# Kernel tuning notes

Hardware: AMD Instinct MI355X
Metric: run time of the kernel (lower is better)

## Reference

```python
import jax, jax.numpy as jnp
import numpy as np

N = 8192      # number of graph nodes (superpixels)
C = 128       # input_dim
OUT = 128     # output_dim
T = 256       # theta_1 projection dim
EPS = 1e-5    # BatchNorm1d eps (default)
NEG = -9e15   # zero_vec fill value from the torch code
SLOPE = 0.01  # LeakyReLU default negative slope


def setup_inputs() -> dict:
    key = jax.random.key(0)
    k = jax.random.split(key, 6)
    H = jax.random.normal(k[0], (N, C), dtype=jnp.float32)
    A = (jax.random.uniform(k[1], (N, N)) < 0.01).astype(jnp.float32)
    gamma = jnp.ones((C,), jnp.float32)
    beta = jnp.zeros((C,), jnp.float32)
    W1 = jax.random.normal(k[2], (C, T), dtype=jnp.float32) * 0.05
    b1 = jnp.zeros((T,), jnp.float32)
    Wo = jax.random.normal(k[3], (C, OUT), dtype=jnp.float32) * 0.05
    bo = jnp.zeros((OUT,), jnp.float32)
    return {"H": H, "A": A, "gamma": gamma, "beta": beta,
            "W1": W1, "b1": b1, "Wo": Wo, "bo": bo}


def _leaky(x):
    return jnp.where(x >= 0, x, SLOPE * x)


def reference(H, A, gamma, beta, W1, b1, Wo, bo):
    # BatchNorm1d (training-mode batch statistics, biased variance)
    mu = H.mean(axis=0)
    var = H.var(axis=0)
    Hn = (H - mu) * jax.lax.rsqrt(var + EPS) * gamma + beta   # [N, C]

    # theta_1 projection and dense pairwise similarity
    Hx = Hn @ W1 + b1                                          # [N, T]
    e = jax.nn.sigmoid(Hx @ Hx.T)                              # [N, N]

    mask = jnp.ceil(A * 1e-5)                                  # 1 where A>0
    A1 = jnp.where(mask > 0, e, jnp.float32(NEG))              # [N, N]

    # model == 'normal' -> no clamp branch
    A_soft = jax.nn.softmax(A1 + jnp.eye(N, dtype=A1.dtype), axis=1)

    HW = Hn @ Wo + bo                                          # [N, OUT]
    out1 = _leaky(A_soft @ HW)
    A1_soft = jax.nn.softmax(A1, axis=1)
    out2 = _leaky(A1_soft @ HW)
    return (out1 + out2, A_soft)
```

## Files before the change

### kernel.cpp

```cpp
#include <hip/hip_runtime.h>


#define NN    8192
#define CC    128
#define TT    256
#define OUTD  128
#define FD    384
#define CAP   256

#define WS_STATS  8
#define WS_PARAMS 264
#define WS_BCAT   520
#define WS_WCAT   904
#define WS_F      50176

typedef unsigned int v4u __attribute__((ext_vector_type(4)));

__device__ __forceinline__ float b2f(unsigned short u) {
    return __uint_as_float(((unsigned int)u) << 16);
}
__device__ __forceinline__ unsigned short f2b(float f) {
    unsigned int x = __float_as_uint(f);
    return (unsigned short)((x + 0x7fffu + ((x >> 16) & 1u)) >> 16);
}
__device__ __forceinline__ int pick_gamma(const void* g0, const void* g1, const void* g2) {
    if (*(const unsigned int*)g0 == 0x3F800000u) return 0;
    if (*(const unsigned int*)g1 == 0x3F800000u) return 1;
    if (*(const unsigned int*)g2 == 0x3F800000u) return 2;
    return 0;
}

__global__ __launch_bounds__(384) void k_init(const float* __restrict__ W1,
                                              const float* __restrict__ b1,
                                              const float* __restrict__ Wo,
                                              const void* g0, const void* g1, const void* g2,
                                              float* __restrict__ ws) {
    int t = threadIdx.x, b = blockIdx.x;
    if (b < 128) {
        ws[WS_WCAT + b * FD + t] = (t < TT) ? W1[(size_t)b * TT + t]
                                            : Wo[(size_t)b * OUTD + (t - TT)];
    } else {
        if (t < 256) ws[WS_STATS + t] = 0.0f;
        int gs = pick_gamma(g0, g1, g2);
        const float* cand[3] = {(const float*)g0, (const float*)g1, (const float*)g2};
        const float* bo = cand[gs == 2 ? 1 : 2];
        ws[WS_BCAT + t] = (t < TT) ? b1[t] : bo[t - TT];
    }
}

__global__ __launch_bounds__(256) void k_stats(const float* __restrict__ H,
                                               float* __restrict__ ws) {
    __shared__ float ssum[256], ssq[256];
    int tid = threadIdx.x;
    int c = tid & 127, rh = tid >> 7;
    int r0 = blockIdx.x * 64;
    float s = 0.0f, q = 0.0f;
#pragma unroll 8
    for (int k = 0; k < 32; ++k) {
        float v = H[(size_t)(r0 + rh + 2 * k) * CC + c];
        s += v; q += v * v;
    }
    ssum[tid] = s; ssq[tid] = q;
    __syncthreads();
    if (tid < 128) {
        atomicAdd(&ws[WS_STATS + c],       ssum[tid] + ssum[tid + 128]);
        atomicAdd(&ws[WS_STATS + 128 + c], ssq[tid]  + ssq[tid + 128]);
    }
}

__global__ __launch_bounds__(128) void k_final(const void* g0, const void* g1, const void* g2,
                                               float* __restrict__ ws) {
    int gs = pick_gamma(g0, g1, g2);
    const float* cand[3] = {(const float*)g0, (const float*)g1, (const float*)g2};
    const float* gamma = cand[gs];
    const float* beta  = cand[gs == 0 ? 1 : 0];
    int c = threadIdx.x;
    float mu  = ws[WS_STATS + c] * (1.0f / NN);
    float var = ws[WS_STATS + 128 + c] * (1.0f / NN) - mu * mu;
    float rs  = rsqrtf(var + 1e-5f);
    float sc  = gamma[c] * rs;
    ws[WS_PARAMS + c]       = sc;
    ws[WS_PARAMS + 128 + c] = beta[c] - mu * sc;
}

__global__ __launch_bounds__(256) void k_gemm(const float* __restrict__ H,
                                              float* __restrict__ ws) {
    __shared__ float As[64][65];
    __shared__ float Bs[64][64];
    const float* params = ws + WS_PARAMS;
    const float* Wcat   = ws + WS_WCAT;
    const float* bcat   = ws + WS_BCAT;
    unsigned short* F   = (unsigned short*)(ws + WS_F);
    int tid = threadIdx.x;
    int m0 = blockIdx.x * 64, n0 = blockIdx.y * 64;
    int ty = tid >> 4, tx = tid & 15;
    float acc[4][4];
#pragma unroll
    for (int m = 0; m < 4; ++m)
#pragma unroll
        for (int n = 0; n < 4; ++n) acc[m][n] = 0.0f;

    for (int ks = 0; ks < CC; ks += 64) {
#pragma unroll
        for (int it = 0; it < 16; ++it) {
            int idx = tid + it * 256;
            int r = idx >> 6, k = idx & 63;
            As[r][k] = H[(size_t)(m0 + r) * CC + ks + k] * params[ks + k]
                     + params[128 + ks + k];
        }
#pragma unroll
        for (int it = 0; it < 16; ++it) {
            int idx = tid + it * 256;
            int k = idx >> 6, n = idx & 63;
            Bs[k][n] = Wcat[(ks + k) * FD + n0 + n];
        }
        __syncthreads();
#pragma unroll
        for (int k = 0; k < 64; ++k) {
            float4 b4 = *(const float4*)&Bs[k][tx * 4];
            float a0 = As[ty * 4 + 0][k];
            float a1 = As[ty * 4 + 1][k];
            float a2 = As[ty * 4 + 2][k];
            float a3 = As[ty * 4 + 3][k];
            acc[0][0] += a0 * b4.x; acc[0][1] += a0 * b4.y; acc[0][2] += a0 * b4.z; acc[0][3] += a0 * b4.w;
            acc[1][0] += a1 * b4.x; acc[1][1] += a1 * b4.y; acc[1][2] += a1 * b4.z; acc[1][3] += a1 * b4.w;
            acc[2][0] += a2 * b4.x; acc[2][1] += a2 * b4.y; acc[2][2] += a2 * b4.z; acc[2][3] += a2 * b4.w;
            acc[3][0] += a3 * b4.x; acc[3][1] += a3 * b4.y; acc[3][2] += a3 * b4.z; acc[3][3] += a3 * b4.w;
        }
        __syncthreads();
    }
#pragma unroll
    for (int n = 0; n < 4; ++n) {
        int gn = n0 + tx * 4 + n;
        float bias = bcat[gn];
#pragma unroll
        for (int m = 0; m < 4; ++m) {
            int gm = m0 + ty * 4 + m;
            F[(size_t)gm * FD + gn] = f2b(acc[m][n] + bias);
        }
    }
}

__global__ __launch_bounds__(256, 8) void k_sattn(const float* __restrict__ A,
                                                  float* __restrict__ ws,
                                                  float* __restrict__ outO,
                                                  float* __restrict__ outAs) {
    __shared__ __align__(16) float hxi[TT];
    __shared__ unsigned short nbr[CAP];
    __shared__ float ev1[CAP];
    __shared__ float ev2[CAP];
    __shared__ float po1[256], po2[256];
    __shared__ int   cnt;
    __shared__ float s1, s2;

    const unsigned short* F = (const unsigned short*)(ws + WS_F);
    int tid = threadIdx.x;
    int i = blockIdx.x;

    const v4u* arow = (const v4u*)(A + (size_t)i * NN);
    v4u r[8];
#pragma unroll
    for (int q = 0; q < 8; ++q) r[q] = arow[tid + 256 * q];

    hxi[tid] = b2f(F[(size_t)i * FD + tid]);
    if (tid == 0) { cnt = 0; s1 = 0.0f; s2 = 0.0f; }
    __syncthreads();

#pragma unroll
    for (int q = 0; q < 8; ++q) {
        if (r[q].x | r[q].y | r[q].z | r[q].w) {
            int base = (tid + 256 * q) * 4;
            if (r[q].x) { int p = atomicAdd(&cnt, 1); if (p < CAP) nbr[p] = (unsigned short)(base + 0); }
            if (r[q].y) { int p = atomicAdd(&cnt, 1); if (p < CAP) nbr[p] = (unsigned short)(base + 1); }
            if (r[q].z) { int p = atomicAdd(&cnt, 1); if (p < CAP) nbr[p] = (unsigned short)(base + 2); }
            if (r[q].w) { int p = atomicAdd(&cnt, 1); if (p < CAP) nbr[p] = (unsigned short)(base + 3); }
        }
    }
    __syncthreads();
    int cn = cnt < CAP ? cnt : CAP;

    int wave = tid >> 6, lane = tid & 63;
    float4 x4 = ((const float4*)hxi)[lane];
    for (int p0 = wave; p0 < cn; p0 += 16) {
        int pp0 = p0, pp1 = p0 + 4, pp2 = p0 + 8, pp3 = p0 + 12;
        ushort4 h0, h1, h2, h3;
        h0 = ((const ushort4*)(F + (size_t)nbr[pp0] * FD))[lane];
        if (pp1 < cn) h1 = ((const ushort4*)(F + (size_t)nbr[pp1] * FD))[lane];
        if (pp2 < cn) h2 = ((const ushort4*)(F + (size_t)nbr[pp2] * FD))[lane];
        if (pp3 < cn) h3 = ((const ushort4*)(F + (size_t)nbr[pp3] * FD))[lane];
        float d0 = b2f(h0.x) * x4.x + b2f(h0.y) * x4.y + b2f(h0.z) * x4.z + b2f(h0.w) * x4.w;
        float d1 = (pp1 < cn) ? b2f(h1.x) * x4.x + b2f(h1.y) * x4.y + b2f(h1.z) * x4.z + b2f(h1.w) * x4.w : 0.0f;
        float d2 = (pp2 < cn) ? b2f(h2.x) * x4.x + b2f(h2.y) * x4.y + b2f(h2.z) * x4.z + b2f(h2.w) * x4.w : 0.0f;
        float d3 = (pp3 < cn) ? b2f(h3.x) * x4.x + b2f(h3.y) * x4.y + b2f(h3.z) * x4.z + b2f(h3.w) * x4.w : 0.0f;
#pragma unroll
        for (int off = 32; off >= 1; off >>= 1) {
            d0 += __shfl_xor(d0, off, 64);
            d1 += __shfl_xor(d1, off, 64);
            d2 += __shfl_xor(d2, off, 64);
            d3 += __shfl_xor(d3, off, 64);
        }
        if (lane == 0) {
            ev1[pp0] = 1.0f / (1.0f + __expf(-d0));
            if (pp1 < cn) ev1[pp1] = 1.0f / (1.0f + __expf(-d1));
            if (pp2 < cn) ev1[pp2] = 1.0f / (1.0f + __expf(-d2));
            if (pp3 < cn) ev1[pp3] = 1.0f / (1.0f + __expf(-d3));
        }
    }
    __syncthreads();

    float l1 = 0.0f, l2 = 0.0f;
    if (tid < cn) {
        float e  = ev1[tid];
        float eb = __expf(e);
        float a1 = ((int)nbr[tid] == i) ? eb * 2.7182818284590452f : eb;
        ev1[tid] = a1; ev2[tid] = eb;
        l1 = a1; l2 = eb;
    }
#pragma unroll
    for (int off = 32; off >= 1; off >>= 1) {
        l1 += __shfl_xor(l1, off, 64);
        l2 += __shfl_xor(l2, off, 64);
    }
    if (lane == 0) { atomicAdd(&s1, l1); atomicAdd(&s2, l2); }
    __syncthreads();

    float inv1 = (s1 > 0.0f) ? 1.0f / s1 : 0.0f;
    float inv2 = (s2 > 0.0f) ? 1.0f / s2 : 0.0f;

    if (tid < cn) outAs[(size_t)i * NN + nbr[tid]] = ev1[tid] * inv1;

    {
        int half = tid >> 7;
        int c = tid & 127;
        const unsigned short* Fhw = F + TT + c;
        float a1 = 0.0f, a2 = 0.0f;
#pragma unroll 8
        for (int p = half; p < cn; p += 2) {
            float h = b2f(Fhw[(size_t)nbr[p] * FD]);
            a1 += ev1[p] * h;
            a2 += ev2[p] * h;
        }
        po1[tid] = a1; po2[tid] = a2;
    }
    __syncthreads();
    if (tid < OUTD) {
        float o1 = (po1[tid] + po1[tid + 128]) * inv1;
        float o2 = (po2[tid] + po2[tid + 128]) * inv2;
        o1 = (o1 >= 0.0f) ? o1 : 0.01f * o1;
        o2 = (o2 >= 0.0f) ? o2 : 0.01f * o2;
        outO[(size_t)i * OUTD + tid] = o1 + o2;
    }
}

extern "C" void kernel_launch(void* const* d_in, const int* in_sizes, int n_in,
                              void* d_out, int out_size, void* d_ws, size_t ws_size,
                              hipStream_t stream) {
    int iH = -1, iA = -1, iW1 = -1, iWo = -1, ib1 = -1, i128[3] = {-1, -1, -1};
    int n128 = 0;
    bool ok = (n_in == 8);
    if (ok) {
        for (int i = 0; i < 8; ++i) {
            int s = in_sizes[i];
            if      (s == 67108864 && iA  < 0) iA  = i;
            else if (s == 1048576  && iH  < 0) iH  = i;
            else if (s == 32768    && iW1 < 0) iW1 = i;
            else if (s == 16384    && iWo < 0) iWo = i;
            else if (s == 256      && ib1 < 0) ib1 = i;
            else if (s == 128      && n128 < 3) i128[n128++] = i;
            else { ok = false; break; }
        }
        if (iA < 0 || iH < 0 || iW1 < 0 || iWo < 0 || ib1 < 0 || n128 != 3) ok = false;
    }
    if (!ok) { iH = 0; iA = 1; i128[0] = 2; i128[1] = 3; iW1 = 4; ib1 = 5; iWo = 6; i128[2] = 7; }

    const float* H  = (const float*)d_in[iH];
    const float* A  = (const float*)d_in[iA];
    const float* W1 = (const float*)d_in[iW1];
    const float* b1 = (const float*)d_in[ib1];
    const float* Wo = (const float*)d_in[iWo];
    const void*  g0 = d_in[i128[0]];
    const void*  g1 = d_in[i128[1]];
    const void*  g2 = d_in[i128[2]];

    float* outO  = (float*)d_out;
    float* outAs = outO + (size_t)NN * OUTD;
    float* ws    = (float*)d_ws;

    k_init <<<129, 384, 0, stream>>>(W1, b1, Wo, g0, g1, g2, ws);
    k_stats<<<128, 256, 0, stream>>>(H, ws);
    k_final<<<1, 128, 0, stream>>>(g0, g1, g2, ws);
    k_gemm <<<dim3(128, 6), 256, 0, stream>>>(H, ws);
    hipMemsetAsync(outAs, 0, (size_t)NN * NN * sizeof(float), stream);
    k_sattn<<<NN, 256, 0, stream>>>(A, ws, outO, outAs);
}
```

Baseline: 528.9 us.

## Process four rows per block and prefetch next adjacency row during compute

The attention kernel now handles four consecutive rows per block instead of one, with a grid of N/4 blocks. Right after building the neighbour list for the current row, it issues the loads of the next row of A, so that 32KB read overlaps the gather and dot-product phase. The cost is fewer blocks (2048), an extra barrier per row, and registers held live across the loop, which can reduce overlap from occupancy. The kernel is likely dominated by streaming the 256MB A matrix and memsetting outAs, so the gain depends on whether per-block latency was the limit.

```diff
diff --git a/kernel.cpp b/kernel.cpp
--- a/kernel.cpp
+++ b/kernel.cpp
@@ -7,6 +7,8 @@
 #define OUTD  128
 #define FD    384
 #define CAP   256
+#define RPB   4
+#define GRID  (NN / RPB)
 
 #define WS_STATS  8
 #define WS_PARAMS 264
@@ -155,100 +157,112 @@
 
     const unsigned short* F = (const unsigned short*)(ws + WS_F);
     int tid = threadIdx.x;
-    int i = blockIdx.x;
-
-    const v4u* arow = (const v4u*)(A + (size_t)i * NN);
+    int base = blockIdx.x * RPB;
+
     v4u r[8];
-#pragma unroll
-    for (int q = 0; q < 8; ++q) r[q] = arow[tid + 256 * q];
-
-    hxi[tid] = b2f(F[(size_t)i * FD + tid]);
-    if (tid == 0) { cnt = 0; s1 = 0.0f; s2 = 0.0f; }
-    __syncthreads();
-
-#pragma unroll
-    for (int q = 0; q < 8; ++q) {
-        if (r[q].x | r[q].y | r[q].z | r[q].w) {
-            int base = (tid + 256 * q) * 4;
-            if (r[q].x) { int p = atomicAdd(&cnt, 1); if (p < CAP) nbr[p] = (unsigned short)(base + 0); }
-            if (r[q].y) { int p = atomicAdd(&cnt, 1); if (p < CAP) nbr[p] = (unsigned short)(base + 1); }
-            if (r[q].z) { int p = atomicAdd(&cnt, 1); if (p < CAP) nbr[p] = (unsigned short)(base + 2); }
-            if (r[q].w) { int p = atomicAdd(&cnt, 1); if (p < CAP) nbr[p] = (unsigned short)(base + 3); }
-        }
-    }
-    __syncthreads();
-    int cn = cnt < CAP ? cnt : CAP;
-
-    int wave = tid >> 6, lane = tid & 63;
-    float4 x4 = ((const float4*)hxi)[lane];
-    for (int p0 = wave; p0 < cn; p0 += 16) {
-        int pp0 = p0, pp1 = p0 + 4, pp2 = p0 + 8, pp3 = p0 + 12;
-        ushort4 h0, h1, h2, h3;
-        h0 = ((const ushort4*)(F + (size_t)nbr[pp0] * FD))[lane];
-        if (pp1 < cn) h1 = ((const ushort4*)(F + (size_t)nbr[pp1] * FD))[lane];
-        if (pp2 < cn) h2 = ((const ushort4*)(F + (size_t)nbr[pp2] * FD))[lane];
-        if (pp3 < cn) h3 = ((const ushort4*)(F + (size_t)nbr[pp3] * FD))[lane];
-        float d0 = b2f(h0.x) * x4.x + b2f(h0.y) * x4.y + b2f(h0.z) * x4.z + b2f(h0.w) * x4.w;
-        float d1 = (pp1 < cn) ? b2f(h1.x) * x4.x + b2f(h1.y) * x4.y + b2f(h1.z) * x4.z + b2f(h1.w) * x4.w : 0.0f;
-        float d2 = (pp2 < cn) ? b2f(h2.x) * x4.x + b2f(h2.y) * x4.y + b2f(h2.z) * x4.z + b2f(h2.w) * x4.w : 0.0f;
-        float d3 = (pp3 < cn) ? b2f(h3.x) * x4.x + b2f(h3.y) * x4.y + b2f(h3.z) * x4.z + b2f(h3.w) * x4.w : 0.0f;
+    {
+        const v4u* a0 = (const v4u*)(A + (size_t)base * NN);
+#pragma unroll
+        for (int q = 0; q < 8; ++q) r[q] = a0[tid + 256 * q];
+    }
+
+    for (int rr = 0; rr < RPB; ++rr) {
+        int i = base + rr;
+        if (tid == 0) { cnt = 0; s1 = 0.0f; s2 = 0.0f; }
+        hxi[tid] = b2f(F[(size_t)i * FD + tid]);
+        __syncthreads();
+
+#pragma unroll
+        for (int q = 0; q < 8; ++q) {
+            if (r[q].x | r[q].y | r[q].z | r[q].w) {
+                int bpos = (tid + 256 * q) * 4;
+                if (r[q].x) { int p = atomicAdd(&cnt, 1); if (p < CAP) nbr[p] = (unsigned short)(bpos + 0); }
+                if (r[q].y) { int p = atomicAdd(&cnt, 1); if (p < CAP) nbr[p] = (unsigned short)(bpos + 1); }
+                if (r[q].z) { int p = atomicAdd(&cnt, 1); if (p < CAP) nbr[p] = (unsigned short)(bpos + 2); }
+                if (r[q].w) { int p = atomicAdd(&cnt, 1); if (p < CAP) nbr[p] = (unsigned short)(bpos + 3); }
+            }
+        }
+        __syncthreads();
+        int cn = cnt < CAP ? cnt : CAP;
+
+        if (rr + 1 < RPB) {
+            const v4u* an = (const v4u*)(A + (size_t)(i + 1) * NN);
+#pragma unroll
+            for (int q = 0; q < 8; ++q) r[q] = an[tid + 256 * q];
+        }
+
+        int wave = tid >> 6, lane = tid & 63;
+        float4 x4 = ((const float4*)hxi)[lane];
+        for (int p0 = wave; p0 < cn; p0 += 16) {
+            int pp1 = p0 + 4, pp2 = p0 + 8, pp3 = p0 + 12;
+            ushort4 h0, h1, h2, h3;
+            h0 = ((const ushort4*)(F + (size_t)nbr[p0] * FD))[lane];
+            if (pp1 < cn) h1 = ((const ushort4*)(F + (size_t)nbr[pp1] * FD))[lane];
+            if (pp2 < cn) h2 = ((const ushort4*)(F + (size_t)nbr[pp2] * FD))[lane];
+            if (pp3 < cn) h3 = ((const ushort4*)(F + (size_t)nbr[pp3] * FD))[lane];
+            float d0 = b2f(h0.x) * x4.x + b2f(h0.y) * x4.y + b2f(h0.z) * x4.z + b2f(h0.w) * x4.w;
+            float d1 = (pp1 < cn) ? b2f(h1.x) * x4.x + b2f(h1.y) * x4.y + b2f(h1.z) * x4.z + b2f(h1.w) * x4.w : 0.0f;
+            float d2 = (pp2 < cn) ? b2f(h2.x) * x4.x + b2f(h2.y) * x4.y + b2f(h2.z) * x4.z + b2f(h2.w) * x4.w : 0.0f;
+            float d3 = (pp3 < cn) ? b2f(h3.x) * x4.x + b2f(h3.y) * x4.y + b2f(h3.z) * x4.z + b2f(h3.w) * x4.w : 0.0f;
+#pragma unroll
+            for (int off = 32; off >= 1; off >>= 1) {
+                d0 += __shfl_xor(d0, off, 64);
+                d1 += __shfl_xor(d1, off, 64);
+                d2 += __shfl_xor(d2, off, 64);
+                d3 += __shfl_xor(d3, off, 64);
+            }
+            if (lane == 0) {
+                ev1[p0] = 1.0f / (1.0f + __expf(-d0));
+                if (pp1 < cn) ev1[pp1] = 1.0f / (1.0f + __expf(-d1));
+                if (pp2 < cn) ev1[pp2] = 1.0f / (1.0f + __expf(-d2));
+                if (pp3 < cn) ev1[pp3] = 1.0f / (1.0f + __expf(-d3));
+            }
+        }
+        __syncthreads();
+
+        float l1 = 0.0f, l2 = 0.0f;
+        if (tid < cn) {
+            float e  = ev1[tid];
+            float eb = __expf(e);
+            float a1 = ((int)nbr[tid] == i) ? eb * 2.7182818284590452f : eb;
+            ev1[tid] = a1; ev2[tid] = eb;
+            l1 = a1; l2 = eb;
+        }
 #pragma unroll
         for (int off = 32; off >= 1; off >>= 1) {
-            d0 += __shfl_xor(d0, off, 64);
-            d1 += __shfl_xor(d1, off, 64);
-            d2 += __shfl_xor(d2, off, 64);
-            d3 += __shfl_xor(d3, off, 64);
-        }
-        if (lane == 0) {
-            ev1[pp0] = 1.0f / (1.0f + __expf(-d0));
-            if (pp1 < cn) ev1[pp1] = 1.0f / (1.0f + __expf(-d1));
-            if (pp2 < cn) ev1[pp2] = 1.0f / (1.0f + __expf(-d2));
-            if (pp3 < cn) ev1[pp3] = 1.0f / (1.0f + __expf(-d3));
-        }
-    }
-    __syncthreads();
-
-    float l1 = 0.0f, l2 = 0.0f;
-    if (tid < cn) {
-        float e  = ev1[tid];
-        float eb = __expf(e);
-        float a1 = ((int)nbr[tid] == i) ? eb * 2.7182818284590452f : eb;
-        ev1[tid] = a1; ev2[tid] = eb;
-        l1 = a1; l2 = eb;
-    }
-#pragma unroll
-    for (int off = 32; off >= 1; off >>= 1) {
-        l1 += __shfl_xor(l1, off, 64);
-        l2 += __shfl_xor(l2, off, 64);
-    }
-    if (lane == 0) { atomicAdd(&s1, l1); atomicAdd(&s2, l2); }
-    __syncthreads();
-
-    float inv1 = (s1 > 0.0f) ? 1.0f / s1 : 0.0f;
-    float inv2 = (s2 > 0.0f) ? 1.0f / s2 : 0.0f;
-
-    if (tid < cn) outAs[(size_t)i * NN + nbr[tid]] = ev1[tid] * inv1;
-
-    {
-        int half = tid >> 7;
-        int c = tid & 127;
-        const unsigned short* Fhw = F + TT + c;
-        float a1 = 0.0f, a2 = 0.0f;
+            l1 += __shfl_xor(l1, off, 64);
+            l2 += __shfl_xor(l2, off, 64);
+        }
+        if (lane == 0) { atomicAdd(&s1, l1); atomicAdd(&s2, l2); }
+        __syncthreads();
+
+        float inv1 = (s1 > 0.0f) ? 1.0f / s1 : 0.0f;
+        float inv2 = (s2 > 0.0f) ? 1.0f / s2 : 0.0f;
+
+        if (tid < cn) outAs[(size_t)i * NN + nbr[tid]] = ev1[tid] * inv1;
+
+        {
+            int half = tid >> 7;
+            int c = tid & 127;
+            const unsigned short* Fhw = F + TT + c;
+            float a1 = 0.0f, a2 = 0.0f;
 #pragma unroll 8
-        for (int p = half; p < cn; p += 2) {
-            float h = b2f(Fhw[(size_t)nbr[p] * FD]);
-            a1 += ev1[p] * h;
-            a2 += ev2[p] * h;
-        }
-        po1[tid] = a1; po2[tid] = a2;
-    }
-    __syncthreads();
-    if (tid < OUTD) {
-        float o1 = (po1[tid] + po1[tid + 128]) * inv1;
-        float o2 = (po2[tid] + po2[tid + 128]) * inv2;
-        o1 = (o1 >= 0.0f) ? o1 : 0.01f * o1;
-        o2 = (o2 >= 0.0f) ? o2 : 0.01f * o2;
-        outO[(size_t)i * OUTD + tid] = o1 + o2;
+            for (int p = half; p < cn; p += 2) {
+                float h = b2f(Fhw[(size_t)nbr[p] * FD]);
+                a1 += ev1[p] * h;
+                a2 += ev2[p] * h;
+            }
+            po1[tid] = a1; po2[tid] = a2;
+        }
+        __syncthreads();
+        if (tid < OUTD) {
+            float o1 = (po1[tid] + po1[tid + 128]) * inv1;
+            float o2 = (po2[tid] + po2[tid + 128]) * inv2;
+            o1 = (o1 >= 0.0f) ? o1 : 0.01f * o1;
+            o2 = (o2 >= 0.0f) ? o2 : 0.01f * o2;
+            outO[(size_t)i * OUTD + tid] = o1 + o2;
+        }
+        __syncthreads();
     }
 }
 
@@ -291,5 +305,5 @@
     k_final<<<1, 128, 0, stream>>>(g0, g1, g2, ws);
     k_gemm <<<dim3(128, 6), 256, 0, stream>>>(H, ws);
     hipMemsetAsync(outAs, 0, (size_t)NN * NN * sizeof(float), stream);
-    k_sattn<<<NN, 256, 0, stream>>>(A, ws, outO, outAs);
-}
+    k_sattn<<<GRID, 256, 0, stream>>>(A, ws, outO, outAs);
+}
```

After: 623.8 us. 17.9% more time.

## Process one graph row per wavefront in sparse attention kernel

Applied to the files above, without the earlier changes.

Restructures the sparse attention kernel so each 64-lane wave handles a whole row independently, with four rows per block. This removes the block-wide __syncthreads barriers and shared-memory atomics on the softmax sums, using wave shuffles instead. The weighted aggregation now has each lane produce two output columns with packed 32-bit loads. The trade-off is less parallelism per row, so each wave scans a full 32 KB row of A and walks every neighbor serially, which may lengthen per-row latency.

```diff
diff --git a/kernel.cpp b/kernel.cpp
--- a/kernel.cpp
+++ b/kernel.cpp
@@ -145,53 +145,53 @@
                                                   float* __restrict__ ws,
                                                   float* __restrict__ outO,
                                                   float* __restrict__ outAs) {
-    __shared__ __align__(16) float hxi[TT];
-    __shared__ unsigned short nbr[CAP];
-    __shared__ float ev1[CAP];
-    __shared__ float ev2[CAP];
-    __shared__ float po1[256], po2[256];
-    __shared__ int   cnt;
-    __shared__ float s1, s2;
+    __shared__ unsigned short nbr[4][CAP];
+    __shared__ float ev1[4][CAP];
+    __shared__ float ev2[4][CAP];
+    __shared__ int   cnt[4][16];
 
     const unsigned short* F = (const unsigned short*)(ws + WS_F);
-    int tid = threadIdx.x;
-    int i = blockIdx.x;
+    int tid  = threadIdx.x;
+    int wv   = tid >> 6, lane = tid & 63;
+    int i    = blockIdx.x * 4 + wv;
+
+    ushort4 hx = ((const ushort4*)(F + (size_t)i * FD))[lane];
+    float4 x4;
+    x4.x = b2f(hx.x); x4.y = b2f(hx.y); x4.z = b2f(hx.z); x4.w = b2f(hx.w);
+
+    if (lane == 0) cnt[wv][0] = 0;
 
     const v4u* arow = (const v4u*)(A + (size_t)i * NN);
-    v4u r[8];
-#pragma unroll
-    for (int q = 0; q < 8; ++q) r[q] = arow[tid + 256 * q];
-
-    hxi[tid] = b2f(F[(size_t)i * FD + tid]);
-    if (tid == 0) { cnt = 0; s1 = 0.0f; s2 = 0.0f; }
-    __syncthreads();
-
-#pragma unroll
-    for (int q = 0; q < 8; ++q) {
-        if (r[q].x | r[q].y | r[q].z | r[q].w) {
-            int base = (tid + 256 * q) * 4;
-            if (r[q].x) { int p = atomicAdd(&cnt, 1); if (p < CAP) nbr[p] = (unsigned short)(base + 0); }
-            if (r[q].y) { int p = atomicAdd(&cnt, 1); if (p < CAP) nbr[p] = (unsigned short)(base + 1); }
-            if (r[q].z) { int p = atomicAdd(&cnt, 1); if (p < CAP) nbr[p] = (unsigned short)(base + 2); }
-            if (r[q].w) { int p = atomicAdd(&cnt, 1); if (p < CAP) nbr[p] = (unsigned short)(base + 3); }
-        }
-    }
-    __syncthreads();
-    int cn = cnt < CAP ? cnt : CAP;
-
-    int wave = tid >> 6, lane = tid & 63;
-    float4 x4 = ((const float4*)hxi)[lane];
-    for (int p0 = wave; p0 < cn; p0 += 16) {
-        int pp0 = p0, pp1 = p0 + 4, pp2 = p0 + 8, pp3 = p0 + 12;
+#pragma unroll
+    for (int ch = 0; ch < 4; ++ch) {
+        v4u r[8];
+#pragma unroll
+        for (int q = 0; q < 8; ++q) r[q] = arow[lane + 64 * q + 512 * ch];
+#pragma unroll
+        for (int q = 0; q < 8; ++q) {
+            if (r[q].x | r[q].y | r[q].z | r[q].w) {
+                int base = (lane + 64 * q + 512 * ch) * 4;
+                if (r[q].x) { int p = atomicAdd(&cnt[wv][0], 1); if (p < CAP) nbr[wv][p] = (unsigned short)(base + 0); }
+                if (r[q].y) { int p = atomicAdd(&cnt[wv][0], 1); if (p < CAP) nbr[wv][p] = (unsigned short)(base + 1); }
+                if (r[q].z) { int p = atomicAdd(&cnt[wv][0], 1); if (p < CAP) nbr[wv][p] = (unsigned short)(base + 2); }
+                if (r[q].w) { int p = atomicAdd(&cnt[wv][0], 1); if (p < CAP) nbr[wv][p] = (unsigned short)(base + 3); }
+            }
+        }
+    }
+    int cn = cnt[wv][0];
+    if (cn > CAP) cn = CAP;
+
+    for (int p0 = 0; p0 < cn; p0 += 4) {
+        int p1 = p0 + 1, p2 = p0 + 2, p3 = p0 + 3;
         ushort4 h0, h1, h2, h3;
-        h0 = ((const ushort4*)(F + (size_t)nbr[pp0] * FD))[lane];
-        if (pp1 < cn) h1 = ((const ushort4*)(F + (size_t)nbr[pp1] * FD))[lane];
-        if (pp2 < cn) h2 = ((const ushort4*)(F + (size_t)nbr[pp2] * FD))[lane];
-        if (pp3 < cn) h3 = ((const ushort4*)(F + (size_t)nbr[pp3] * FD))[lane];
+        h0 = ((const ushort4*)(F + (size_t)nbr[wv][p0] * FD))[lane];
+        if (p1 < cn) h1 = ((const ushort4*)(F + (size_t)nbr[wv][p1] * FD))[lane];
+        if (p2 < cn) h2 = ((const ushort4*)(F + (size_t)nbr[wv][p2] * FD))[lane];
+        if (p3 < cn) h3 = ((const ushort4*)(F + (size_t)nbr[wv][p3] * FD))[lane];
         float d0 = b2f(h0.x) * x4.x + b2f(h0.y) * x4.y + b2f(h0.z) * x4.z + b2f(h0.w) * x4.w;
-        float d1 = (pp1 < cn) ? b2f(h1.x) * x4.x + b2f(h1.y) * x4.y + b2f(h1.z) * x4.z + b2f(h1.w) * x4.w : 0.0f;
-        float d2 = (pp2 < cn) ? b2f(h2.x) * x4.x + b2f(h2.y) * x4.y + b2f(h2.z) * x4.z + b2f(h2.w) * x4.w : 0.0f;
-        float d3 = (pp3 < cn) ? b2f(h3.x) * x4.x + b2f(h3.y) * x4.y + b2f(h3.z) * x4.z + b2f(h3.w) * x4.w : 0.0f;
+        float d1 = (p1 < cn) ? b2f(h1.x) * x4.x + b2f(h1.y) * x4.y + b2f(h1.z) * x4.z + b2f(h1.w) * x4.w : 0.0f;
+        float d2 = (p2 < cn) ? b2f(h2.x) * x4.x + b2f(h2.y) * x4.y + b2f(h2.z) * x4.z + b2f(h2.w) * x4.w : 0.0f;
+        float d3 = (p3 < cn) ? b2f(h3.x) * x4.x + b2f(h3.y) * x4.y + b2f(h3.z) * x4.z + b2f(h3.w) * x4.w : 0.0f;
 #pragma unroll
         for (int off = 32; off >= 1; off >>= 1) {
             d0 += __shfl_xor(d0, off, 64);
@@ -200,55 +200,53 @@
             d3 += __shfl_xor(d3, off, 64);
         }
         if (lane == 0) {
-            ev1[pp0] = 1.0f / (1.0f + __expf(-d0));
-            if (pp1 < cn) ev1[pp1] = 1.0f / (1.0f + __expf(-d1));
-            if (pp2 < cn) ev1[pp2] = 1.0f / (1.0f + __expf(-d2));
-            if (pp3 < cn) ev1[pp3] = 1.0f / (1.0f + __expf(-d3));
-        }
-    }
-    __syncthreads();
+            ev1[wv][p0] = 1.0f / (1.0f + __expf(-d0));
+            if (p1 < cn) ev1[wv][p1] = 1.0f / (1.0f + __expf(-d1));
+            if (p2 < cn) ev1[wv][p2] = 1.0f / (1.0f + __expf(-d2));
+            if (p3 < cn) ev1[wv][p3] = 1.0f / (1.0f + __expf(-d3));
+        }
+    }
 
     float l1 = 0.0f, l2 = 0.0f;
-    if (tid < cn) {
-        float e  = ev1[tid];
+    for (int p = lane; p < cn; p += 64) {
+        float e  = ev1[wv][p];
         float eb = __expf(e);
-        float a1 = ((int)nbr[tid] == i) ? eb * 2.7182818284590452f : eb;
-        ev1[tid] = a1; ev2[tid] = eb;
-        l1 = a1; l2 = eb;
+        float a1 = ((int)nbr[wv][p] == i) ? eb * 2.7182818284590452f : eb;
+        ev1[wv][p] = a1; ev2[wv][p] = eb;
+        l1 += a1; l2 += eb;
     }
 #pragma unroll
     for (int off = 32; off >= 1; off >>= 1) {
         l1 += __shfl_xor(l1, off, 64);
         l2 += __shfl_xor(l2, off, 64);
     }
-    if (lane == 0) { atomicAdd(&s1, l1); atomicAdd(&s2, l2); }
-    __syncthreads();
-
-    float inv1 = (s1 > 0.0f) ? 1.0f / s1 : 0.0f;
-    float inv2 = (s2 > 0.0f) ? 1.0f / s2 : 0.0f;
-
-    if (tid < cn) outAs[(size_t)i * NN + nbr[tid]] = ev1[tid] * inv1;
+    float inv1 = (l1 > 0.0f) ? 1.0f / l1 : 0.0f;
+    float inv2 = (l2 > 0.0f) ? 1.0f / l2 : 0.0f;
+
+    for (int p = lane; p < cn; p += 64) {
+        outAs[(size_t)i * NN + nbr[wv][p]] = ev1[wv][p] * inv1;
+    }
 
     {
-        int half = tid >> 7;
-        int c = tid & 127;
-        const unsigned short* Fhw = F + TT + c;
-        float a1 = 0.0f, a2 = 0.0f;
-#pragma unroll 8
-        for (int p = half; p < cn; p += 2) {
-            float h = b2f(Fhw[(size_t)nbr[p] * FD]);
-            a1 += ev1[p] * h;
-            a2 += ev2[p] * h;
-        }
-        po1[tid] = a1; po2[tid] = a2;
-    }
-    __syncthreads();
-    if (tid < OUTD) {
-        float o1 = (po1[tid] + po1[tid + 128]) * inv1;
-        float o2 = (po2[tid] + po2[tid + 128]) * inv2;
-        o1 = (o1 >= 0.0f) ? o1 : 0.01f * o1;
-        o2 = (o2 >= 0.0f) ? o2 : 0.01f * o2;
-        outO[(size_t)i * OUTD + tid] = o1 + o2;
+        const unsigned short* Ft = F + TT + 2 * lane;
+        float a1a = 0.0f, a1b = 0.0f, a2a = 0.0f, a2b = 0.0f;
+#pragma unroll 4
+        for (int p = 0; p < cn; ++p) {
+            unsigned int hh = *(const unsigned int*)(Ft + (size_t)nbr[wv][p] * FD);
+            float h0 = b2f((unsigned short)(hh & 0xffffu));
+            float h1 = b2f((unsigned short)(hh >> 16));
+            float w1 = ev1[wv][p], w2 = ev2[wv][p];
+            a1a += w1 * h0; a1b += w1 * h1;
+            a2a += w2 * h0; a2b += w2 * h1;
+        }
+        float o1a = a1a * inv1, o1b = a1b * inv1;
+        float o2a = a2a * inv2, o2b = a2b * inv2;
+        o1a = (o1a >= 0.0f) ? o1a : 0.01f * o1a;
+        o1b = (o1b >= 0.0f) ? o1b : 0.01f * o1b;
+        o2a = (o2a >= 0.0f) ? o2a : 0.01f * o2a;
+        o2b = (o2b >= 0.0f) ? o2b : 0.01f * o2b;
+        float2 o; o.x = o1a + o2a; o.y = o1b + o2b;
+        *(float2*)(outO + (size_t)i * OUTD + 2 * lane) = o;
     }
 }
 
@@ -291,5 +289,5 @@
     k_final<<<1, 128, 0, stream>>>(g0, g1, g2, ws);
     k_gemm <<<dim3(128, 6), 256, 0, stream>>>(H, ws);
     hipMemsetAsync(outAs, 0, (size_t)NN * NN * sizeof(float), stream);
-    k_sattn<<<NN, 256, 0, stream>>>(A, ws, outO, outAs);
-}
+    k_sattn<<<NN / 4, 256, 0, stream>>>(A, ws, outO, outAs);
+}
```

Result: slower. 541.4 us (+2.3%).
